# Performance work log

Hardware: AMD Instinct MI355X
Metric: run time of the kernel (lower is better)

## Reference

```python
import jax, jax.numpy as jnp
import numpy as np

B, T, D, C = 64, 512, 768, 31  # batch, bert seq len, hidden size, num clause boundaries


def setup_inputs() -> dict:
    key = jax.random.key(0)
    k1, k2, k3 = jax.random.split(key, 3)
    hidden_state = jax.random.normal(k1, (B, T, D), dtype=jnp.float32)
    # Strictly increasing clause-end token positions in (0, T): evenly spaced base + jitter
    step = T // (C + 1)  # 16
    base = (jnp.arange(1, C + 1) * step)[None, :]                       # [1, C]
    jitter = jax.random.randint(k2, (B, C), 0, step - 1)                # < step => strictly increasing
    clause_b = (base + jitter).astype(jnp.int32)                        # [B, C]
    w5 = jax.random.normal(k3, (D, 1), dtype=jnp.float32) * 0.02        # fc5 weight
    b5 = jnp.zeros((1,), dtype=jnp.float32)                             # fc5 bias
    return {"hidden_state": hidden_state, "clause_b": clause_b, "w5": w5, "b5": b5}


def reference(hidden_state, clause_b, w5, b5):
    # Per-clause variable-length softmax-attention pooling over BERT hidden states.
    # Segment j of batch b covers tokens [starts[b,j], ends[b,j]).
    Bq, Tq, Dq = hidden_state.shape
    scores = (hidden_state @ w5).squeeze(-1) + b5[0]                    # [B, T]  (fc5)
    starts = jnp.concatenate(
        [jnp.zeros((Bq, 1), clause_b.dtype), clause_b], axis=1)        # [B, C+1]
    ends = jnp.concatenate(
        [clause_b, jnp.full((Bq, 1), Tq, clause_b.dtype)], axis=1)     # [B, C+1]
    t = jnp.arange(Tq)
    mask = (t[None, None, :] >= starts[:, :, None]) & \
           (t[None, None, :] < ends[:, :, None])                       # [B, C+1, T]
    neg = jnp.asarray(-1e30, dtype=scores.dtype)
    s = jnp.where(mask, scores[:, None, :], neg)
    w = jax.nn.softmax(s, axis=-1)                                      # [B, C+1, T]
    doc_sents_h = jnp.einsum('bjt,btd->bjd', w, hidden_state)           # [B, C+1, D]
    return doc_sents_h
```

## Files before the change

kernel.cpp:

```cpp
#include <hip/hip_runtime.h>


#define B_ 64
#define T_ 512
#define D_ 768
#define C_ 31
#define NSEG 32

__global__ __launch_bounds__(192) void seg_softmax_pool(
    const float* __restrict__ hidden,
    const int*   __restrict__ clause_b,
    const float* __restrict__ w5,
    const float* __restrict__ b5,
    float*       __restrict__ out)
{
    const int blk  = blockIdx.x;
    const int b    = blk >> 5;
    const int j    = blk & 31;
    const int tid  = threadIdx.x;
    const int wave = tid >> 6;
    const int lane = tid & 63;

    const int start = (j == 0)  ? 0  : clause_b[b * C_ + j - 1];
    const int end   = (j == C_) ? T_ : clause_b[b * C_ + j];
    const int L     = end - start;

    __shared__ float s_scores[T_];

    const float* hseg = hidden + ((size_t)b * T_ + start) * D_;

    const float4 wv0 = *(const float4*)(w5 + 4 * lane);
    const float4 wv1 = *(const float4*)(w5 + 4 * lane + 256);
    const float4 wv2 = *(const float4*)(w5 + 4 * lane + 512);
    const float  bias = b5[0];

    for (int t = wave; t < L; t += 3) {
        const float* hp = hseg + (size_t)t * D_;
        const float4 h0 = *(const float4*)(hp + 4 * lane);
        const float4 h1 = *(const float4*)(hp + 4 * lane + 256);
        const float4 h2 = *(const float4*)(hp + 4 * lane + 512);
        float p = h0.x * wv0.x + h0.y * wv0.y + h0.z * wv0.z + h0.w * wv0.w
                + h1.x * wv1.x + h1.y * wv1.y + h1.z * wv1.z + h1.w * wv1.w
                + h2.x * wv2.x + h2.y * wv2.y + h2.z * wv2.z + h2.w * wv2.w;
        #pragma unroll
        for (int off = 32; off > 0; off >>= 1)
            p += __shfl_xor(p, off, 64);
        if (lane == 0) s_scores[t] = p + bias;
    }
    __syncthreads();

    float m = -INFINITY;
    for (int t = 0; t < L; ++t) m = fmaxf(m, s_scores[t]);
    float denom = 0.0f;
    for (int t = 0; t < L; ++t) denom += __expf(s_scores[t] - m);
    const float inv = 1.0f / denom;

    float4 acc = make_float4(0.f, 0.f, 0.f, 0.f);
    const float* hp = hseg + 4 * tid;
    for (int t = 0; t < L; ++t) {
        const float  w = __expf(s_scores[t] - m);
        const float4 h = *(const float4*)(hp + (size_t)t * D_);
        acc.x += w * h.x;
        acc.y += w * h.y;
        acc.z += w * h.z;
        acc.w += w * h.w;
    }
    acc.x *= inv; acc.y *= inv; acc.z *= inv; acc.w *= inv;

    float4* op = (float4*)(out + ((size_t)b * NSEG + j) * D_ + 4 * tid);
    *op = acc;
}

extern "C" void kernel_launch(void* const* d_in, const int* in_sizes, int n_in,
                              void* d_out, int out_size, void* d_ws, size_t ws_size,
                              hipStream_t stream) {
    const float* hidden   = (const float*)d_in[0];
    const int*   clause_b = (const int*)d_in[1];
    const float* w5       = (const float*)d_in[2];
    const float* b5       = (const float*)d_in[3];
    float*       out      = (float*)d_out;

    const int nblocks = B_ * NSEG;
    seg_softmax_pool<<<nblocks, 192, 0, stream>>>(hidden, clause_b, w5, b5, out);
}
```

Baseline: 165.3 us.

## Fuse score and pooling passes with online softmax, one wave per segment

Replaces the two-pass design (score tokens into shared memory, then re-read hidden states to pool) with a single pass per wave that computes each token's score and folds it into an online-softmax running accumulator. Each segment's hidden rows are then read from global memory once instead of twice, and the block-wide sync and shared scratch are removed. Each wave handles a whole segment with 12 floats per lane and a one-row register prefetch, packing four segments per 256-thread block. In exchange each token step now runs a serial dependency chain of a wave reduction plus two exps, parallelism per segment drops to one wave, and the grid shrinks fourfold.

```diff
diff --git a/kernel.cpp b/kernel.cpp
--- a/kernel.cpp
+++ b/kernel.cpp
@@ -7,68 +7,75 @@
 #define C_ 31
 #define NSEG 32
 
-__global__ __launch_bounds__(192) void seg_softmax_pool(
+__global__ __launch_bounds__(256) void seg_softmax_pool_online(
     const float* __restrict__ hidden,
     const int*   __restrict__ clause_b,
     const float* __restrict__ w5,
     const float* __restrict__ b5,
     float*       __restrict__ out)
 {
-    const int blk  = blockIdx.x;
-    const int b    = blk >> 5;
-    const int j    = blk & 31;
-    const int tid  = threadIdx.x;
-    const int wave = tid >> 6;
-    const int lane = tid & 63;
+    const int wave = threadIdx.x >> 6;
+    const int lane = threadIdx.x & 63;
+    const int seg  = blockIdx.x * 4 + wave;
+    const int b    = seg >> 5;
+    const int j    = seg & 31;
 
     const int start = (j == 0)  ? 0  : clause_b[b * C_ + j - 1];
     const int end   = (j == C_) ? T_ : clause_b[b * C_ + j];
     const int L     = end - start;
 
-    __shared__ float s_scores[T_];
+    const int doff = 4 * lane;
+    const float4 w0 = *(const float4*)(w5 + doff);
+    const float4 w1 = *(const float4*)(w5 + doff + 256);
+    const float4 w2 = *(const float4*)(w5 + doff + 512);
+    const float bias = b5[0];
 
-    const float* hseg = hidden + ((size_t)b * T_ + start) * D_;
+    const float* hseg = hidden + ((size_t)b * T_ + start) * D_ + doff;
 
-    const float4 wv0 = *(const float4*)(w5 + 4 * lane);
-    const float4 wv1 = *(const float4*)(w5 + 4 * lane + 256);
-    const float4 wv2 = *(const float4*)(w5 + 4 * lane + 512);
-    const float  bias = b5[0];
+    float4 a0 = make_float4(0.f, 0.f, 0.f, 0.f);
+    float4 a1 = a0, a2 = a0;
+    float m = -INFINITY, denom = 0.0f;
 
-    for (int t = wave; t < L; t += 3) {
-        const float* hp = hseg + (size_t)t * D_;
-        const float4 h0 = *(const float4*)(hp + 4 * lane);
-        const float4 h1 = *(const float4*)(hp + 4 * lane + 256);
-        const float4 h2 = *(const float4*)(hp + 4 * lane + 512);
-        float p = h0.x * wv0.x + h0.y * wv0.y + h0.z * wv0.z + h0.w * wv0.w
-                + h1.x * wv1.x + h1.y * wv1.y + h1.z * wv1.z + h1.w * wv1.w
-                + h2.x * wv2.x + h2.y * wv2.y + h2.z * wv2.z + h2.w * wv2.w;
+    float4 c0 = *(const float4*)(hseg);
+    float4 c1 = *(const float4*)(hseg + 256);
+    float4 c2 = *(const float4*)(hseg + 512);
+
+    for (int t = 0; t < L; ++t) {
+        float4 n0 = make_float4(0.f, 0.f, 0.f, 0.f), n1 = n0, n2 = n0;
+        if (t + 1 < L) {
+            const float* np = hseg + (size_t)(t + 1) * D_;
+            n0 = *(const float4*)(np);
+            n1 = *(const float4*)(np + 256);
+            n2 = *(const float4*)(np + 512);
+        }
+
+        float p = c0.x * w0.x + c0.y * w0.y + c0.z * w0.z + c0.w * w0.w
+                + c1.x * w1.x + c1.y * w1.y + c1.z * w1.z + c1.w * w1.w
+                + c2.x * w2.x + c2.y * w2.y + c2.z * w2.z + c2.w * w2.w;
         #pragma unroll
         for (int off = 32; off > 0; off >>= 1)
             p += __shfl_xor(p, off, 64);
-        if (lane == 0) s_scores[t] = p + bias;
+        const float s = p + bias;
+
+        const float mn    = fmaxf(m, s);
+        const float scale = __expf(m - mn);
+        const float e     = __expf(s - mn);
+        denom = denom * scale + e;
+        a0.x = a0.x * scale + e * c0.x;  a0.y = a0.y * scale + e * c0.y;
+        a0.z = a0.z * scale + e * c0.z;  a0.w = a0.w * scale + e * c0.w;
+        a1.x = a1.x * scale + e * c1.x;  a1.y = a1.y * scale + e * c1.y;
+        a1.z = a1.z * scale + e * c1.z;  a1.w = a1.w * scale + e * c1.w;
+        a2.x = a2.x * scale + e * c2.x;  a2.y = a2.y * scale + e * c2.y;
+        a2.z = a2.z * scale + e * c2.z;  a2.w = a2.w * scale + e * c2.w;
+        m = mn;
+        c0 = n0; c1 = n1; c2 = n2;
     }
-    __syncthreads();
 
-    float m = -INFINITY;
-    for (int t = 0; t < L; ++t) m = fmaxf(m, s_scores[t]);
-    float denom = 0.0f;
-    for (int t = 0; t < L; ++t) denom += __expf(s_scores[t] - m);
     const float inv = 1.0f / denom;
-
-    float4 acc = make_float4(0.f, 0.f, 0.f, 0.f);
-    const float* hp = hseg + 4 * tid;
-    for (int t = 0; t < L; ++t) {
-        const float  w = __expf(s_scores[t] - m);
-        const float4 h = *(const float4*)(hp + (size_t)t * D_);
-        acc.x += w * h.x;
-        acc.y += w * h.y;
-        acc.z += w * h.z;
-        acc.w += w * h.w;
-    }
-    acc.x *= inv; acc.y *= inv; acc.z *= inv; acc.w *= inv;
-
-    float4* op = (float4*)(out + ((size_t)b * NSEG + j) * D_ + 4 * tid);
-    *op = acc;
+    float* op = out + ((size_t)b * NSEG + j) * D_ + doff;
+    *(float4*)(op)       = make_float4(a0.x * inv, a0.y * inv, a0.z * inv, a0.w * inv);
+    *(float4*)(op + 256) = make_float4(a1.x * inv, a1.y * inv, a1.z * inv, a1.w * inv);
+    *(float4*)(op + 512) = make_float4(a2.x * inv, a2.y * inv, a2.z * inv, a2.w * inv);
 }
 
 extern "C" void kernel_launch(void* const* d_in, const int* in_sizes, int n_in,
@@ -80,6 +87,5 @@
     const float* b5       = (const float*)d_in[3];
     float*       out      = (float*)d_out;
 
-    const int nblocks = B_ * NSEG;
-    seg_softmax_pool<<<nblocks, 192, 0, stream>>>(hidden, clause_b, w5, b5, out);
+    seg_softmax_pool_online<<<B_ * NSEG / 4, 256, 0, stream>>>(hidden, clause_b, w5, b5, out);
 }
```

After: 161.3 us. 1.03x faster.
